# Kernel optimization log

Measured on AMD Instinct MI355X. Metric: run time of the kernel, lower is better.

## Reference

```python
import jax, jax.numpy as jnp
import numpy as np

N_QUBITS = 4
N_LAYERS = 2
BATCH = 524288
TWO_PI = 6.283185307179586


def _bc(m):
    # broadcast a per-batch scalar [B] (or python/0-d scalar) over the 3
    # remaining qubit axes after one qubit axis has been taken out
    m = jnp.asarray(m)
    return m.reshape(m.shape + (1, 1, 1)) if m.ndim == 1 else m


def apply_1q(state, q, m00, m01, m10, m11):
    # state: [B,2,2,2,2] complex64; qubit q lives on axis q+1
    ax = q + 1
    a0 = jnp.take(state, 0, axis=ax)  # [B,2,2,2]
    a1 = jnp.take(state, 1, axis=ax)
    n0 = _bc(m00) * a0 + _bc(m01) * a1
    n1 = _bc(m10) * a0 + _bc(m11) * a1
    return jnp.stack([n0, n1], axis=ax)


def apply_cnot(state, c, t):
    ca, ta = c + 1, t + 1
    s0 = jnp.take(state, 0, axis=ca)
    s1 = jnp.take(state, 1, axis=ca)
    ta2 = ta - 1 if ta > ca else ta  # target axis index after removing control axis
    s1 = jnp.flip(s1, axis=ta2)      # X on target within control=1 subspace
    return jnp.stack([s0, s1], axis=ca)


def _circuit(inputs, angles):
    B = inputs.shape[0]
    state = jnp.zeros((B,) + (2,) * N_QUBITS, dtype=jnp.complex64)
    state = state.at[:, 0, 0, 0, 0].set(1.0)

    # AngleEmbedding: RX(x_q) on each wire (PennyLane default rotation='X')
    for q in range(N_QUBITS):
        th = inputs[:, q].astype(jnp.float32) * 0.5
        c = jnp.cos(th).astype(jnp.complex64)
        s = (-1j) * jnp.sin(th).astype(jnp.complex64)
        state = apply_1q(state, q, c, s, s, c)

    # 2 entangling layers: RY, RZ per wire, then CNOT chain + ring closure
    for layer in range(N_LAYERS):
        for q in range(N_QUBITS):
            ty = angles[layer, q, 0] * 0.5
            cy = jnp.cos(ty).astype(jnp.complex64)
            sy = jnp.sin(ty).astype(jnp.complex64)
            state = apply_1q(state, q, cy, -sy, sy, cy)
            tz = angles[layer, q, 1] * 0.5
            ez = jnp.exp(1j * tz.astype(jnp.complex64))
            state = apply_1q(state, q, jnp.conj(ez), 0.0, 0.0, ez)
        for q in range(N_QUBITS - 1):
            state = apply_cnot(state, q, q + 1)
        state = apply_cnot(state, N_QUBITS - 1, 0)

    # <Z_q> = P(bit_q=0) - P(bit_q=1)
    probs = jnp.abs(state) ** 2  # float32 [B,2,2,2,2]
    exps = []
    for q in range(N_QUBITS):
        p0 = jnp.take(probs, 0, axis=q + 1).sum(axis=(1, 2, 3))
        p1 = jnp.take(probs, 1, axis=q + 1).sum(axis=(1, 2, 3))
        exps.append(p0 - p1)
    return jnp.stack(exps, axis=-1).astype(jnp.float32)  # [B,4]


def setup_inputs() -> dict:
    key = jax.random.key(0)
    k1, k2 = jax.random.split(key)
    inputs = jax.random.uniform(k1, (BATCH, N_QUBITS), dtype=jnp.float32) * TWO_PI
    angles = jax.random.uniform(k2, (N_LAYERS, N_QUBITS, 2), dtype=jnp.float32) * TWO_PI
    return {"inputs": inputs, "angles": angles}


def reference(inputs, angles):
    return _circuit(inputs, angles)
```

## Files before the change

kernel.cpp:

```cpp
#include <hip/hip_runtime.h>

static __global__ void prep_consts(const float* __restrict__ angles,
                                   float* __restrict__ cst) {
    int g = threadIdx.x;
    if (g < 8) {
        int layer = g >> 2, q = g & 3;
        float ty = angles[(layer * 4 + q) * 2 + 0] * 0.5f;
        float tz = angles[(layer * 4 + q) * 2 + 1] * 0.5f;
        float cy, sy, cz, sz;
        sincosf(ty, &sy, &cy);
        sincosf(tz, &sz, &cz);
        float* m = cst + g * 8;
        m[0] = cy * cz;  m[1] = -cy * sz;
        m[2] = -sy * cz; m[3] = sy * sz;
        m[4] = sy * cz;  m[5] = sy * sz;
        m[6] = cy * cz;  m[7] = cy * sz;
    }
}

template <int CM, int TM>
static __device__ __forceinline__ void cnot16(float (&ar)[16], float (&ai)[16]) {
#pragma unroll
    for (int i = 0; i < 16; ++i) {
        if ((i & CM) && !(i & TM)) {
            const int j = i | TM;
            float tr = ar[i]; ar[i] = ar[j]; ar[j] = tr;
            float ti = ai[i]; ai[i] = ai[j]; ai[j] = ti;
        }
    }
}

template <int TM>
static __device__ __forceinline__ void gate16(float (&ar)[16], float (&ai)[16],
                                              float m0, float m1, float m2, float m3,
                                              float m4, float m5, float m6, float m7) {
#pragma unroll
    for (int i = 0; i < 16; ++i) {
        if (!(i & TM)) {
            const int j = i | TM;
            const float a0r = ar[i], a0i = ai[i];
            const float a1r = ar[j], a1i = ai[j];
            ar[i] = m0 * a0r - m1 * a0i + m2 * a1r - m3 * a1i;
            ai[i] = m0 * a0i + m1 * a0r + m2 * a1i + m3 * a1r;
            ar[j] = m4 * a0r - m5 * a0i + m6 * a1r - m7 * a1i;
            ai[j] = m4 * a0i + m5 * a0r + m6 * a1i + m7 * a1r;
        }
    }
}

__launch_bounds__(256)
static __global__ void qsim4(const float4* __restrict__ in,
                             const float* __restrict__ cst,
                             float4* __restrict__ out, int B) {
    const int b = blockIdx.x * 256 + threadIdx.x;
    if (b >= B) return;

    const float4 x = in[b];
    float c[4], s[4];
    __sincosf(x.x * 0.5f, &s[0], &c[0]);
    __sincosf(x.y * 0.5f, &s[1], &c[1]);
    __sincosf(x.z * 0.5f, &s[2], &c[2]);
    __sincosf(x.w * 0.5f, &s[3], &c[3]);

    float vr[4][2], vi[4][2];
#pragma unroll
    for (int q = 0; q < 4; ++q) {
        const float m0 = cst[q * 8 + 0], m1 = cst[q * 8 + 1];
        const float m2 = cst[q * 8 + 2], m3 = cst[q * 8 + 3];
        const float m4 = cst[q * 8 + 4], m5 = cst[q * 8 + 5];
        const float m6 = cst[q * 8 + 6], m7 = cst[q * 8 + 7];
        vr[q][0] = m0 * c[q] + m3 * s[q];
        vi[q][0] = m1 * c[q] - m2 * s[q];
        vr[q][1] = m4 * c[q] + m7 * s[q];
        vi[q][1] = m5 * c[q] - m6 * s[q];
    }

    float w01r[4], w01i[4], w23r[4], w23i[4];
#pragma unroll
    for (int j = 0; j < 4; ++j) {
        const int h = j >> 1, l = j & 1;
        w01r[j] = vr[0][h] * vr[1][l] - vi[0][h] * vi[1][l];
        w01i[j] = vr[0][h] * vi[1][l] + vi[0][h] * vr[1][l];
        w23r[j] = vr[2][h] * vr[3][l] - vi[2][h] * vi[3][l];
        w23i[j] = vr[2][h] * vi[3][l] + vi[2][h] * vr[3][l];
    }
    float ar[16], ai[16];
#pragma unroll
    for (int i = 0; i < 16; ++i) {
        const int h = i >> 2, l = i & 3;
        ar[i] = w01r[h] * w23r[l] - w01i[h] * w23i[l];
        ai[i] = w01r[h] * w23i[l] + w01i[h] * w23r[l];
    }

    cnot16<8, 4>(ar, ai);
    cnot16<4, 2>(ar, ai);
    cnot16<2, 1>(ar, ai);
    cnot16<1, 8>(ar, ai);

#pragma unroll
    for (int q = 0; q < 4; ++q) {
        const float* m = cst + (4 + q) * 8;
        const float m0 = m[0], m1 = m[1], m2 = m[2], m3 = m[3];
        const float m4 = m[4], m5 = m[5], m6 = m[6], m7 = m[7];
        if (q == 0) gate16<8>(ar, ai, m0, m1, m2, m3, m4, m5, m6, m7);
        if (q == 1) gate16<4>(ar, ai, m0, m1, m2, m3, m4, m5, m6, m7);
        if (q == 2) gate16<2>(ar, ai, m0, m1, m2, m3, m4, m5, m6, m7);
        if (q == 3) gate16<1>(ar, ai, m0, m1, m2, m3, m4, m5, m6, m7);
    }
    cnot16<8, 4>(ar, ai);
    cnot16<4, 2>(ar, ai);
    cnot16<2, 1>(ar, ai);
    cnot16<1, 8>(ar, ai);

    float p[16];
#pragma unroll
    for (int i = 0; i < 16; ++i) p[i] = ar[i] * ar[i] + ai[i] * ai[i];

    float e0 = 0.f, e1 = 0.f, e2 = 0.f, e3 = 0.f;
#pragma unroll
    for (int i = 0; i < 16; ++i) {
        e0 += (i & 8) ? -p[i] : p[i];
        e1 += (i & 4) ? -p[i] : p[i];
        e2 += (i & 2) ? -p[i] : p[i];
        e3 += (i & 1) ? -p[i] : p[i];
    }

    out[b] = make_float4(e0, e1, e2, e3);
}

extern "C" void kernel_launch(void* const* d_in, const int* in_sizes, int n_in,
                              void* d_out, int out_size, void* d_ws, size_t ws_size,
                              hipStream_t stream) {
    const float* inputs = (const float*)d_in[0];
    const float* angles = (const float*)d_in[1];
    float* cst = (float*)d_ws;
    const int B = in_sizes[0] / 4;

    prep_consts<<<1, 64, 0, stream>>>(angles, cst);
    qsim4<<<(B + 255) / 256, 256, 0, stream>>>((const float4*)inputs, cst,
                                               (float4*)d_out, B);
}
```

Before: 75.56 us.

## Fold constant prep into main kernel and drop last-layer RZ gates

Removes the separate constant-preparation kernel. Each thread now computes the angle sines and cosines itself with fast intrinsics, which saves one launch and the dependency between the two kernels. The last layer's RZ gates are dropped: they are diagonal and only permuted by the following CNOTs, so they cannot change the Z-expectation probabilities. That lets the last-layer gates become real-only RY rotations with far fewer FLOPs. The expectation sums are also restructured into a shared pairwise tree, at the cost of redundant per-thread trig on the uniform angles.

```diff
diff --git a/kernel.cpp b/kernel.cpp
--- a/kernel.cpp
+++ b/kernel.cpp
@@ -1,22 +1,5 @@
 #include <hip/hip_runtime.h>
 
-static __global__ void prep_consts(const float* __restrict__ angles,
-                                   float* __restrict__ cst) {
-    int g = threadIdx.x;
-    if (g < 8) {
-        int layer = g >> 2, q = g & 3;
-        float ty = angles[(layer * 4 + q) * 2 + 0] * 0.5f;
-        float tz = angles[(layer * 4 + q) * 2 + 1] * 0.5f;
-        float cy, sy, cz, sz;
-        sincosf(ty, &sy, &cy);
-        sincosf(tz, &sz, &cz);
-        float* m = cst + g * 8;
-        m[0] = cy * cz;  m[1] = -cy * sz;
-        m[2] = -sy * cz; m[3] = sy * sz;
-        m[4] = sy * cz;  m[5] = sy * sz;
-        m[6] = cy * cz;  m[7] = cy * sz;
-    }
-}
 
 template <int CM, int TM>
 static __device__ __forceinline__ void cnot16(float (&ar)[16], float (&ai)[16]) {
@@ -31,48 +14,53 @@
 }
 
 template <int TM>
-static __device__ __forceinline__ void gate16(float (&ar)[16], float (&ai)[16],
-                                              float m0, float m1, float m2, float m3,
-                                              float m4, float m5, float m6, float m7) {
+static __device__ __forceinline__ void ry16(float (&ar)[16], float (&ai)[16],
+                                            float cy, float sy) {
 #pragma unroll
     for (int i = 0; i < 16; ++i) {
         if (!(i & TM)) {
             const int j = i | TM;
             const float a0r = ar[i], a0i = ai[i];
             const float a1r = ar[j], a1i = ai[j];
-            ar[i] = m0 * a0r - m1 * a0i + m2 * a1r - m3 * a1i;
-            ai[i] = m0 * a0i + m1 * a0r + m2 * a1i + m3 * a1r;
-            ar[j] = m4 * a0r - m5 * a0i + m6 * a1r - m7 * a1i;
-            ai[j] = m4 * a0i + m5 * a0r + m6 * a1i + m7 * a1r;
+            ar[i] = cy * a0r - sy * a1r;
+            ai[i] = cy * a0i - sy * a1i;
+            ar[j] = sy * a0r + cy * a1r;
+            ai[j] = sy * a0i + cy * a1i;
         }
     }
 }
 
 __launch_bounds__(256)
 static __global__ void qsim4(const float4* __restrict__ in,
-                             const float* __restrict__ cst,
+                             const float* __restrict__ ang,
                              float4* __restrict__ out, int B) {
     const int b = blockIdx.x * 256 + threadIdx.x;
     if (b >= B) return;
 
+    float c0y[4], s0y[4], c0z[4], s0z[4], c1y[4], s1y[4];
+#pragma unroll
+    for (int q = 0; q < 4; ++q) {
+        __sincosf(ang[q * 2 + 0] * 0.5f, &s0y[q], &c0y[q]);
+        __sincosf(ang[q * 2 + 1] * 0.5f, &s0z[q], &c0z[q]);
+        __sincosf(ang[8 + q * 2 + 0] * 0.5f, &s1y[q], &c1y[q]);
+    }
+
     const float4 x = in[b];
-    float c[4], s[4];
-    __sincosf(x.x * 0.5f, &s[0], &c[0]);
-    __sincosf(x.y * 0.5f, &s[1], &c[1]);
-    __sincosf(x.z * 0.5f, &s[2], &c[2]);
-    __sincosf(x.w * 0.5f, &s[3], &c[3]);
+    float cx[4], sx[4];
+    __sincosf(x.x * 0.5f, &sx[0], &cx[0]);
+    __sincosf(x.y * 0.5f, &sx[1], &cx[1]);
+    __sincosf(x.z * 0.5f, &sx[2], &cx[2]);
+    __sincosf(x.w * 0.5f, &sx[3], &cx[3]);
 
     float vr[4][2], vi[4][2];
 #pragma unroll
     for (int q = 0; q < 4; ++q) {
-        const float m0 = cst[q * 8 + 0], m1 = cst[q * 8 + 1];
-        const float m2 = cst[q * 8 + 2], m3 = cst[q * 8 + 3];
-        const float m4 = cst[q * 8 + 4], m5 = cst[q * 8 + 5];
-        const float m6 = cst[q * 8 + 6], m7 = cst[q * 8 + 7];
-        vr[q][0] = m0 * c[q] + m3 * s[q];
-        vi[q][0] = m1 * c[q] - m2 * s[q];
-        vr[q][1] = m4 * c[q] + m7 * s[q];
-        vi[q][1] = m5 * c[q] - m6 * s[q];
+        const float t0r = c0y[q] * cx[q], t0i = s0y[q] * sx[q];
+        const float t1r = s0y[q] * cx[q], t1i = -c0y[q] * sx[q];
+        vr[q][0] = t0r * c0z[q] + t0i * s0z[q];
+        vi[q][0] = t0i * c0z[q] - t0r * s0z[q];
+        vr[q][1] = t1r * c0z[q] - t1i * s0z[q];
+        vi[q][1] = t1i * c0z[q] + t1r * s0z[q];
     }
 
     float w01r[4], w01i[4], w23r[4], w23i[4];
@@ -97,16 +85,10 @@
     cnot16<2, 1>(ar, ai);
     cnot16<1, 8>(ar, ai);
 
-#pragma unroll
-    for (int q = 0; q < 4; ++q) {
-        const float* m = cst + (4 + q) * 8;
-        const float m0 = m[0], m1 = m[1], m2 = m[2], m3 = m[3];
-        const float m4 = m[4], m5 = m[5], m6 = m[6], m7 = m[7];
-        if (q == 0) gate16<8>(ar, ai, m0, m1, m2, m3, m4, m5, m6, m7);
-        if (q == 1) gate16<4>(ar, ai, m0, m1, m2, m3, m4, m5, m6, m7);
-        if (q == 2) gate16<2>(ar, ai, m0, m1, m2, m3, m4, m5, m6, m7);
-        if (q == 3) gate16<1>(ar, ai, m0, m1, m2, m3, m4, m5, m6, m7);
-    }
+    ry16<8>(ar, ai, c1y[0], s1y[0]);
+    ry16<4>(ar, ai, c1y[1], s1y[1]);
+    ry16<2>(ar, ai, c1y[2], s1y[2]);
+    ry16<1>(ar, ai, c1y[3], s1y[3]);
     cnot16<8, 4>(ar, ai);
     cnot16<4, 2>(ar, ai);
     cnot16<2, 1>(ar, ai);
@@ -116,14 +98,20 @@
 #pragma unroll
     for (int i = 0; i < 16; ++i) p[i] = ar[i] * ar[i] + ai[i] * ai[i];
 
-    float e0 = 0.f, e1 = 0.f, e2 = 0.f, e3 = 0.f;
+    float p2[8], p4[4], p8[2];
 #pragma unroll
-    for (int i = 0; i < 16; ++i) {
-        e0 += (i & 8) ? -p[i] : p[i];
-        e1 += (i & 4) ? -p[i] : p[i];
-        e2 += (i & 2) ? -p[i] : p[i];
-        e3 += (i & 1) ? -p[i] : p[i];
-    }
+    for (int j = 0; j < 8; ++j) p2[j] = p[2 * j] + p[2 * j + 1];
+#pragma unroll
+    for (int j = 0; j < 4; ++j) p4[j] = p2[2 * j] + p2[2 * j + 1];
+    p8[0] = p4[0] + p4[1];
+    p8[1] = p4[2] + p4[3];
+
+    const float e0 = p8[0] - p8[1];
+    const float e1 = (p4[0] - p4[1]) + (p4[2] - p4[3]);
+    const float e2 = (p2[0] - p2[1]) + (p2[2] - p2[3]) + (p2[4] - p2[5]) + (p2[6] - p2[7]);
+    float e3 = 0.f;
+#pragma unroll
+    for (int j = 0; j < 8; ++j) e3 += p[2 * j] - p[2 * j + 1];
 
     out[b] = make_float4(e0, e1, e2, e3);
 }
@@ -133,10 +121,9 @@
                               hipStream_t stream) {
     const float* inputs = (const float*)d_in[0];
     const float* angles = (const float*)d_in[1];
-    float* cst = (float*)d_ws;
     const int B = in_sizes[0] / 4;
+    (void)d_ws; (void)ws_size;
 
-    prep_consts<<<1, 64, 0, stream>>>(angles, cst);
-    qsim4<<<(B + 255) / 256, 256, 0, stream>>>((const float4*)inputs, cst,
+    qsim4<<<(B + 255) / 256, 256, 0, stream>>>((const float4*)inputs, angles,
                                                (float4*)d_out, B);
 }
```

Measured after the change: 65.98 us. 12.7% less time.
